# Performance work log

Hardware: AMD Instinct MI355X
Metric: run time of the kernel (lower is better)

## Reference

```python
import jax, jax.numpy as jnp
import numpy as np

B, T, D = 2, 2048, 1024
H, HKV, HD = 16, 4, 64  # num_heads, num_kv_heads, head_dim
EPS = 1.1920929e-07  # torch.finfo(float32).eps, nn.RMSNorm default


def _rmsnorm(x, g):
    return x * jax.lax.rsqrt(jnp.mean(x * x, axis=-1, keepdims=True) + EPS) * g


def _ternary(w):
    # ternary quantize {-1,0,+1} with straight-through estimator
    th = jnp.mean(jnp.abs(w))
    wt = jnp.sign(w) * (jnp.abs(w) > th).astype(w.dtype)
    return w + jax.lax.stop_gradient(wt - w)


def _bitlinear(x, w, g):
    return _rmsnorm(x, g) @ _ternary(w).T


def setup_inputs() -> dict:
    key = jax.random.key(0)
    ks = jax.random.split(key, 5)
    kaiming = lambda k, shape: jax.random.normal(k, shape, jnp.float32) * np.float32(np.sqrt(2.0 / shape[1]))
    return {
        "x": jax.random.normal(ks[0], (B, T, D), jnp.float32),
        "q_w": kaiming(ks[1], (D, D)),
        "q_g": jnp.ones((D,), jnp.float32),
        "k_w": kaiming(ks[2], (HKV * HD, D)),
        "k_g": jnp.ones((D,), jnp.float32),
        "v_w": kaiming(ks[3], (HKV * HD, D)),
        "o_w": kaiming(ks[4], (D, D)),
        "o_g": jnp.ones((D,), jnp.float32),
        "qk_gain": jnp.float32(5.25),
    }


def reference(x, q_w, q_g, k_w, k_g, v_w, o_w, o_g, qk_gain):
    b, t, d = x.shape
    q = _bitlinear(x, q_w, q_g).reshape(b, t, H, HD)          # [B,T,H,hd]
    k = _bitlinear(x, k_w, k_g).reshape(b, t, HKV, HD)        # [B,T,Hkv,hd]
    v = (x @ v_w.T).reshape(b, t, HKV, HD)                    # [B,T,Hkv,hd]
    rep = H // HKV
    k = jnp.repeat(k, rep, axis=2)                            # GQA expand -> [B,T,H,hd]
    v = jnp.repeat(v, rep, axis=2)
    scale = qk_gain / np.float32(np.sqrt(HD))
    attn = jnp.einsum('bqhd,bkhd->bhqk', q, k) * scale        # [B,H,T,T]
    causal = jnp.tril(jnp.ones((t, t), bool))
    attn = jnp.where(causal, attn, -jnp.inf)
    attn = jax.nn.softmax(attn, axis=-1)
    out = jnp.einsum('bhqk,bkhd->bqhd', attn, v).reshape(b, t, d)
    return _bitlinear(out, o_w, o_g)
```

## Files before the change

kernel.cpp:

```cpp
#include <hip/hip_runtime.h>
#include <hip/hip_bf16.h>
#include <cstdint>
#include <cstddef>

typedef unsigned short u16;
typedef unsigned int u32;
typedef __attribute__((ext_vector_type(8))) short short8v;
typedef __attribute__((ext_vector_type(4))) float f32x4;
typedef __attribute__((ext_vector_type(4))) u16 u16x4;
typedef __attribute__((ext_vector_type(8))) u16 u16x8;

static constexpr int Bc = 2, Tc = 2048, Dc = 1024, Hc = 16, HKVc = 4, HDc = 64;
static constexpr int Mc = Bc * Tc;
static constexpr float EPSc = 1.1920929e-07f;

static __device__ __forceinline__ u16 f2bf(float f) {
  u32 u = __builtin_bit_cast(u32, f);
  return (u16)((u + 0x7fffu + ((u >> 16) & 1u)) >> 16);
}
static __device__ __forceinline__ float bf2f(u16 b) {
  u32 u = ((u32)b) << 16;
  return __builtin_bit_cast(float, u);
}
static __device__ __forceinline__ float fast_exp2(float x) {
  float r;
  asm("v_exp_f32 %0, %1" : "=v"(r) : "v"(x));
  return r;
}
static __device__ __forceinline__ u32 cvt_pk_bf16(float lo, float hi) {
  u32 r;
  asm("v_cvt_pk_bf16_f32 %0, %1, %2" : "=v"(r) : "v"(lo), "v"(hi));
  return r;
}

__global__ __launch_bounds__(256) void np_leafsum_all(const float* __restrict__ q_w,
                                                      const float* __restrict__ k_w,
                                                      const float* __restrict__ o_w,
                                                      float* __restrict__ leaf) {
  int blk = blockIdx.x;
  const float* w;
  float* out;
  int lfbase;
  if (blk < 256)      { w = q_w; out = leaf;         lfbase = blk * 32; }
  else if (blk < 320) { w = k_w; out = leaf + 8192;  lfbase = (blk - 256) * 32; }
  else                { w = o_w; out = leaf + 10240; lfbase = (blk - 320) * 32; }
  int t = threadIdx.x;
  int lf = lfbase + (t >> 3), j = t & 7;
  const float* a = w + (size_t)lf * 128;
  float r = fabsf(a[j]);
#pragma unroll
  for (int i = 8; i < 128; i += 8) r += fabsf(a[i + j]);
  float x = r + __shfl_xor(r, 1);
  float y = x + __shfl_xor(x, 2);
  float z = y + __shfl_xor(y, 4);
  if (j == 0) out[lf] = z;
}

__global__ __launch_bounds__(256) void np_treemean3(const float* __restrict__ leaf,
                                                    float* __restrict__ th) {
  int m = blockIdx.x;
  const float* src = leaf + (m == 0 ? 0 : (m == 1 ? 8192 : 10240));
  int nle = (m == 1) ? 2048 : 8192;
  float inv_n = (m == 1) ? (1.0f / 262144.0f) : (1.0f / 1048576.0f);
  int t = threadIdx.x;
  int chunk = nle >> 8;
  float v[32];
  for (int i = 0; i < chunk; i += 4) {
    float4 f = *(const float4*)&src[t * chunk + i];
    v[i] = f.x; v[i + 1] = f.y; v[i + 2] = f.z; v[i + 3] = f.w;
  }
  for (int cnt = chunk >> 1; cnt >= 1; cnt >>= 1)
    for (int i = 0; i < cnt; ++i) v[i] = v[2 * i] + v[2 * i + 1];
  float s = v[0];
#pragma unroll
  for (int off = 1; off < 64; off <<= 1) s += __shfl_xor(s, off);
  __shared__ float red[4];
  if ((t & 63) == 0) red[t >> 6] = s;
  __syncthreads();
  if (t == 0) th[m] = ((red[0] + red[1]) + (red[2] + red[3])) * inv_n;
}

__global__ __launch_bounds__(256) void quant_split_all(const float* __restrict__ q_w,
                                                       const float* __restrict__ k_w,
                                                       const float* __restrict__ o_w,
                                                       const float* __restrict__ v_w,
                                                       const float* __restrict__ th,
                                                       u16* __restrict__ Wq,
                                                       u16* __restrict__ Wk,
                                                       u16* __restrict__ Wo,
                                                       u16* __restrict__ Vwh) {
  int i4 = blockIdx.x * 256 + threadIdx.x;
  if (i4 < 589824) {
    const float* w; u16* o; float t;
    int j;
    if (i4 < 262144)      { w = q_w; o = Wq; t = th[0]; j = i4; }
    else if (i4 < 327680) { w = k_w; o = Wk; t = th[1]; j = i4 - 262144; }
    else                  { w = o_w; o = Wo; t = th[2]; j = i4 - 327680; }
    float4 v = *(const float4*)&w[(size_t)j * 4];
    float y[4] = {v.x, v.y, v.z, v.w};
    u16x4 q;
#pragma unroll
    for (int c = 0; c < 4; ++c)
      q[c] = (y[c] > t) ? (u16)0x3F80 : ((y[c] < -t) ? (u16)0xBF80 : (u16)0);
    *(u16x4*)&o[(size_t)j * 4] = q;
  } else {
    int j = i4 - 589824;
    float4 v = *(const float4*)&v_w[(size_t)j * 4];
    float y[4] = {v.x, v.y, v.z, v.w};
    u16x4 h;
#pragma unroll
    for (int c = 0; c < 4; ++c) h[c] = f2bf(y[c]);
    *(u16x4*)&Vwh[(size_t)j * 4] = h;
  }
}

__global__ __launch_bounds__(256) void rmsnorm_split6(const float* __restrict__ X,
                                                      const float* __restrict__ g1,
                                                      const float* __restrict__ g2,
                                                      u16* __restrict__ H1, u16* __restrict__ L1,
                                                      u16* __restrict__ H2, u16* __restrict__ L2,
                                                      u16* __restrict__ HV) {
  int row = blockIdx.x;
  const float* xr = X + (size_t)row * Dc;
  int tid = threadIdx.x;
  float4 v = *(const float4*)&xr[tid * 4];
  float vv[4] = {v.x, v.y, v.z, v.w};
  if (HV != nullptr) {
    u16x4 h;
#pragma unroll
    for (int j = 0; j < 4; ++j) h[j] = f2bf(vv[j]);
    *(u16x4*)&HV[(size_t)row * Dc + tid * 4] = h;
  }
  float ss = v.x * v.x + v.y * v.y + v.z * v.z + v.w * v.w;
#pragma unroll
  for (int off = 1; off < 64; off <<= 1) ss += __shfl_xor(ss, off);
  __shared__ float red[4];
  if ((tid & 63) == 0) red[tid >> 6] = ss;
  __syncthreads();
  float tot = red[0] + red[1] + red[2] + red[3];
  float inv = 1.0f / sqrtf(tot * (1.0f / (float)Dc) + EPSc);
  {
    float4 a = *(const float4*)&g1[tid * 4];
    float ga[4] = {a.x, a.y, a.z, a.w};
    u16x4 h, l;
#pragma unroll
    for (int j = 0; j < 4; ++j) {
      float y = vv[j] * inv * ga[j];
      u16 hb = f2bf(y);
      h[j] = hb;
      l[j] = f2bf(y - bf2f(hb));
    }
    *(u16x4*)&H1[(size_t)row * Dc + tid * 4] = h;
    if (L1 != nullptr) *(u16x4*)&L1[(size_t)row * Dc + tid * 4] = l;
  }
  if (g2 != nullptr) {
    float4 a = *(const float4*)&g2[tid * 4];
    float ga[4] = {a.x, a.y, a.z, a.w};
    u16x4 h, l;
#pragma unroll
    for (int j = 0; j < 4; ++j) {
      float y = vv[j] * inv * ga[j];
      u16 hb = f2bf(y);
      h[j] = hb;
      l[j] = f2bf(y - bf2f(hb));
    }
    *(u16x4*)&H2[(size_t)row * Dc + tid * 4] = h;
    if (L2 != nullptr) *(u16x4*)&L2[(size_t)row * Dc + tid * 4] = l;
  }
}

template <bool PA, int MODE>
static __device__ __forceinline__ void gemm_body(
    const u16* __restrict__ Ah, const u16* __restrict__ Al,
    const u16* __restrict__ Bh,
    int N, int K, int bm, int bn,
    float* __restrict__ C, u16* __restrict__ O1, u16* __restrict__ O2,
    u16* smem) {
  constexpr int APT = 2, BPT = 4;
  u16* AhS = smem;
  u16* AlS = smem + 4096;
  u16* BhS = smem + 8192;
  int tid = threadIdx.x;
  int l = tid & 63, w = tid >> 6;
  int wm = (w >> 1) * 32, wn = (w & 1) * 64;
  u16x8 rAh[APT], rAl[PA ? APT : 1], rBh[BPT];
  f32x4 acc[2][4] = {};
#define LOADTILE(kb_)                                                               \
  {                                                                                 \
    _Pragma("unroll") for (int p = 0; p < APT; ++p) {                               \
      int idx = tid + p * 256;                                                      \
      int row = idx >> 3, cc = idx & 7;                                             \
      rAh[p] = *(const u16x8*)&Ah[(size_t)(bm + row) * K + (kb_) + cc * 8];         \
      if (PA) rAl[p] = *(const u16x8*)&Al[(size_t)(bm + row) * K + (kb_) + cc * 8]; \
    }                                                                               \
    _Pragma("unroll") for (int p = 0; p < BPT; ++p) {                               \
      int idx = tid + p * 256;                                                      \
      int row = idx >> 3, cc = idx & 7;                                             \
      rBh[p] = *(const u16x8*)&Bh[(size_t)(bn + row) * K + (kb_) + cc * 8];         \
    }                                                                               \
  }
  LOADTILE(0)
  for (int kb = 0; kb < K; kb += 64) {
    __syncthreads();
#pragma unroll
    for (int p = 0; p < APT; ++p) {
      int idx = tid + p * 256;
      int row = idx >> 3, cc = idx & 7;
      int off = row * 64 + ((cc * 8) ^ ((row & 7) << 3));
      *(u16x8*)&AhS[off] = rAh[p];
      if (PA) *(u16x8*)&AlS[off] = rAl[p];
    }
#pragma unroll
    for (int p = 0; p < BPT; ++p) {
      int idx = tid + p * 256;
      int row = idx >> 3, cc = idx & 7;
      int off = row * 64 + ((cc * 8) ^ ((row & 7) << 3));
      *(u16x8*)&BhS[off] = rBh[p];
    }
    if (kb + 64 < K) LOADTILE(kb + 64)
    __syncthreads();
    __builtin_amdgcn_s_setprio(1);
#pragma unroll
    for (int sl = 0; sl < 2; ++sl) {
      short8v fa[2], fal[2], fb[4];
      int kof = (l >> 4) * 8 + sl * 32;
#pragma unroll
      for (int m = 0; m < 2; ++m) {
        int row = wm + m * 16 + (l & 15);
        int off = row * 64 + (kof ^ ((row & 7) << 3));
        fa[m] = *(const short8v*)&AhS[off];
        if (PA) fal[m] = *(const short8v*)&AlS[off];
      }
#pragma unroll
      for (int n = 0; n < 4; ++n) {
        int row = wn + n * 16 + (l & 15);
        int off = row * 64 + (kof ^ ((row & 7) << 3));
        fb[n] = *(const short8v*)&BhS[off];
      }
#pragma unroll
      for (int m = 0; m < 2; ++m)
#pragma unroll
        for (int n = 0; n < 4; ++n) {
          acc[m][n] = __builtin_amdgcn_mfma_f32_16x16x32_bf16(fa[m], fb[n], acc[m][n], 0, 0, 0);
          if (PA)
            acc[m][n] = __builtin_amdgcn_mfma_f32_16x16x32_bf16(fal[m], fb[n], acc[m][n], 0, 0, 0);
        }
    }
    __builtin_amdgcn_s_setprio(0);
  }
#undef LOADTILE
#pragma unroll
  for (int m = 0; m < 2; ++m)
#pragma unroll
    for (int n = 0; n < 4; ++n)
#pragma unroll
      for (int r = 0; r < 4; ++r) {
        int grow = bm + wm + m * 16 + (l >> 4) * 4 + r;
        int gcol = bn + wn + n * 16 + (l & 15);
        float v = acc[m][n][r];
        if (MODE == 0) {
          C[(size_t)grow * N + gcol] = v;
        } else if (MODE == 1) {
          u16 hb = f2bf(v);
          O1[(size_t)grow * N + gcol] = hb;
          O2[(size_t)grow * N + gcol] = f2bf(v - bf2f(hb));
        } else {
          int k = gcol & 31;
          int gp = (gcol & ~31) | (((k >> 2) & 3) << 3) |
                   (((k >> 4) & 1) << 2) | (k & 3);
          O1[(size_t)grow * N + gp] = f2bf(v);
        }
      }
}

__global__ __launch_bounds__(256, 1) void qkv_mega(
    const u16* __restrict__ Xqh, const u16* __restrict__ Xql, const u16* __restrict__ Wq,
    const u16* __restrict__ Xkh, const u16* __restrict__ Xkl, const u16* __restrict__ Wk,
    const u16* __restrict__ Xvh, const u16* __restrict__ Vwh,
    u16* __restrict__ Qh, u16* __restrict__ Ql,
    u16* __restrict__ Kh, u16* __restrict__ Kl,
    u16* __restrict__ Vt) {
  __shared__ __align__(16) u16 SMEM[16384];
  int bx = blockIdx.x;
  if (bx < 512) {
    int bm = (bx >> 3) * 64, bn = (bx & 7) * 128;
    gemm_body<true, 1>(Xqh, Xql, Wq, 1024, 1024, bm, bn, nullptr, Qh, Ql, SMEM);
  } else if (bx < 640) {
    int t = bx - 512;
    int bm = (t >> 1) * 64, bn = (t & 1) * 128;
    gemm_body<true, 1>(Xkh, Xkl, Wk, 256, 1024, bm, bn, nullptr, Kh, Kl, SMEM);
  } else {
    int t = bx - 640;
    int bm = (t >> 5) * 64, bn = (t & 31) * 128;
    gemm_body<false, 3>(Vwh, nullptr, Xvh, 4096, 1024, bm, bn, nullptr, Vt, nullptr, SMEM);
  }
}

__global__ __launch_bounds__(256, 1) void o_gemm(
    const u16* __restrict__ Ah, const u16* __restrict__ Bh,
    float* __restrict__ C) {
  __shared__ __align__(16) u16 SMEM[16384];
  int bm = blockIdx.y * 64, bn = blockIdx.x * 128;
  gemm_body<false, 0>(Ah, nullptr, Bh, 1024, 1024, bm, bn, C, nullptr, nullptr, SMEM);
}

__global__ __launch_bounds__(256, 3) void attn_part(
    const u16* __restrict__ Qh, const u16* __restrict__ Ql,
    const u16* __restrict__ Kh, const u16* __restrict__ Kl,
    const u16* __restrict__ Vt,
    const float* __restrict__ qk_gain,
    u16* __restrict__ Opart, float* __restrict__ MLpart) {
  __shared__ __align__(16) u16 SM[24576];
  int tid = threadIdx.x;
  int w = tid >> 6, l = tid & 63;
  int hb = blockIdx.x;
  int h = hb & 15, b = hb >> 4;
  int kvh = h >> 2;
  int f = blockIdx.y;
  int qt, ci;
  if (f < 4)       { qt = f; ci = 0; }
  else if (f < 12) { int o = f - 4;  qt = 4 + (o >> 1); ci = o & 1; }
  else if (f < 24) { int o = f - 12; qt = 8 + o / 3;    ci = o - (o / 3) * 3; }
  else             { int o = f - 24; qt = 12 + (o >> 2); ci = o & 3; }
  int q0 = qt * 128;
  int tsteps = 2 * qt + 2;
  int s0 = ci * 8;
  int s1 = (s0 + 8 < tsteps) ? (s0 + 8) : tsteps;
  const float sc2 = qk_gain[0] * 0.125f * 1.44269504f;
  u16x8 pk[2], pl[2], pv[2];
#define AISSUE3(K0)                                                             \
  {                                                                             \
    _Pragma("unroll") for (int p = 0; p < 2; ++p) {                             \
      int idx = tid + p * 256;                                                  \
      int jj = idx >> 3, cc = idx & 7;                                          \
      size_t kb = ((size_t)(b * Tc + (K0) + jj)) * (HKVc * HDc) + kvh * 64 + cc * 8; \
      pk[p] = *(const u16x8*)&Kh[kb];                                           \
      pl[p] = *(const u16x8*)&Kl[kb];                                           \
      size_t vb = ((size_t)(kvh * 64 + jj)) * (size_t)Mc + b * Tc + (K0) + cc * 8; \
      pv[p] = *(const u16x8*)&Vt[vb];                                           \
    }                                                                           \
  }
#define WRITEBUF(BI)                                                            \
  {                                                                             \
    u16* bb = SM + (BI) * 12288;                                                \
    _Pragma("unroll") for (int p = 0; p < 2; ++p) {                             \
      int idx = tid + p * 256;                                                  \
      int jj = idx >> 3, cc = idx & 7;                                          \
      int sw = jj * 64 + ((cc * 8) ^ ((jj & 7) << 3));                          \
      *(u16x8*)&bb[sw] = pk[p];                                                 \
      *(u16x8*)&bb[4096 + sw] = pl[p];                                          \
      *(u16x8*)&bb[8192 + sw] = pv[p];                                          \
    }                                                                           \
  }
  short8v qb_h[4], qb_l[4];
#pragma unroll
  for (int qp = 0; qp < 2; ++qp) {
    size_t qrow = (size_t)(b * Tc + q0 + w * 32 + qp * 16 + (l & 15));
#pragma unroll
    for (int sl = 0; sl < 2; ++sl) {
      int dstart = (l >> 4) * 8 + sl * 32;
      qb_h[qp * 2 + sl] = *(const short8v*)&Qh[qrow * Dc + h * 64 + dstart];
      qb_l[qp * 2 + sl] = *(const short8v*)&Ql[qrow * Dc + h * 64 + dstart];
    }
  }
  f32x4 Oacc[8] = {{0,0,0,0},{0,0,0,0},{0,0,0,0},{0,0,0,0},
                   {0,0,0,0},{0,0,0,0},{0,0,0,0},{0,0,0,0}};
  float mrow[2] = {-3.0e38f, -3.0e38f};
  float lrow[2] = {0.f, 0.f};
  int qmax_w = q0 + w * 32 + 31;
  AISSUE3(s0 * 64)
  WRITEBUF(0)
  if (s0 + 1 < s1) AISSUE3((s0 + 1) * 64)
  __syncthreads();
  for (int li = 0; li < s1 - s0; ++li) {
    int stp = s0 + li;
    int k0 = stp * 64;
    u16* Kh_s = SM + (li & 1) * 12288;
    u16* Kl_s = Kh_s + 4096;
    u16* Vt_s = Kh_s + 8192;
    if (stp + 1 < s1) WRITEBUF((li + 1) & 1)
    if (stp + 2 < s1) AISSUE3((stp + 2) * 64)
    if (k0 <= qmax_w) {
      f32x4 s[8] = {{0,0,0,0},{0,0,0,0},{0,0,0,0},{0,0,0,0},
                    {0,0,0,0},{0,0,0,0},{0,0,0,0},{0,0,0,0}};
      __builtin_amdgcn_s_setprio(1);
#pragma unroll
      for (int kt = 0; kt < 4; ++kt) {
        int key = kt * 16 + (l & 15);
#pragma unroll
        for (int sl = 0; sl < 2; ++sl) {
          int dstart = ((l >> 4) * 8 + 32 * sl) ^ ((key & 7) << 3);
          short8v bh = *(const short8v*)&Kh_s[key * 64 + dstart];
          short8v bl = *(const short8v*)&Kl_s[key * 64 + dstart];
#pragma unroll
          for (int qp = 0; qp < 2; ++qp) {
            s[qp * 4 + kt] = __builtin_amdgcn_mfma_f32_16x16x32_bf16(bh, qb_h[qp * 2 + sl], s[qp * 4 + kt], 0, 0, 0);
            s[qp * 4 + kt] = __builtin_amdgcn_mfma_f32_16x16x32_bf16(bl, qb_h[qp * 2 + sl], s[qp * 4 + kt], 0, 0, 0);
            s[qp * 4 + kt] = __builtin_amdgcn_mfma_f32_16x16x32_bf16(bh, qb_l[qp * 2 + sl], s[qp * 4 + kt], 0, 0, 0);
          }
        }
      }
      __builtin_amdgcn_s_setprio(0);
      bool full = (k0 + 63) <= (q0 + w * 32);
      if (!full) {
#pragma unroll
        for (int qp = 0; qp < 2; ++qp) {
          int qg = q0 + w * 32 + qp * 16 + (l & 15);
#pragma unroll
          for (int kt = 0; kt < 4; ++kt)
#pragma unroll
            for (int r = 0; r < 4; ++r)
              if (k0 + kt * 16 + ((l >> 4) << 2) + r > qg) s[qp * 4 + kt][r] = -3.0e38f;
        }
      }
      float p[2][4][4];
#pragma unroll
      for (int qp = 0; qp < 2; ++qp) {
        float mk[4];
#pragma unroll
        for (int kt = 0; kt < 4; ++kt)
          mk[kt] = fmaxf(fmaxf(s[qp * 4 + kt][0], s[qp * 4 + kt][1]),
                         fmaxf(s[qp * 4 + kt][2], s[qp * 4 + kt][3]));
        float mx = fmaxf(fmaxf(mk[0], mk[1]), fmaxf(mk[2], mk[3]));
        mx = fmaxf(mx, __shfl_xor(mx, 16));
        mx = fmaxf(mx, __shfl_xor(mx, 32));
        float mnew = fmaxf(mrow[qp], mx);
        float msc = mnew * sc2;
        float corr = fast_exp2(__builtin_fmaf(mrow[qp], sc2, -msc));
        mrow[qp] = mnew;
        float sk[4];
#pragma unroll
        for (int kt = 0; kt < 4; ++kt) {
#pragma unroll
          for (int r = 0; r < 4; ++r)
            p[qp][kt][r] = fast_exp2(__builtin_fmaf(s[qp * 4 + kt][r], sc2, -msc));
          sk[kt] = (p[qp][kt][0] + p[qp][kt][1]) + (p[qp][kt][2] + p[qp][kt][3]);
        }
        float rs = (sk[0] + sk[1]) + (sk[2] + sk[3]);
        rs += __shfl_xor(rs, 16);
        rs += __shfl_xor(rs, 32);
        lrow[qp] = lrow[qp] * corr + rs;
#pragma unroll
        for (int dt = 0; dt < 4; ++dt) Oacc[qp * 4 + dt] *= corr;
      }
      short8v fbv[4];
#pragma unroll
      for (int qp = 0; qp < 2; ++qp)
#pragma unroll
        for (int sl = 0; sl < 2; ++sl) {
          union { u32 u[4]; short8v v; } fq;
          fq.u[0] = cvt_pk_bf16(p[qp][2 * sl][0], p[qp][2 * sl][1]);
          fq.u[1] = cvt_pk_bf16(p[qp][2 * sl][2], p[qp][2 * sl][3]);
          fq.u[2] = cvt_pk_bf16(p[qp][2 * sl + 1][0], p[qp][2 * sl + 1][1]);
          fq.u[3] = cvt_pk_bf16(p[qp][2 * sl + 1][2], p[qp][2 * sl + 1][3]);
          fbv[qp * 2 + sl] = fq.v;
        }
      __builtin_amdgcn_s_setprio(1);
#pragma unroll
      for (int dt = 0; dt < 4; ++dt) {
        int d = dt * 16 + (l & 15);
#pragma unroll
        for (int sl = 0; sl < 2; ++sl) {
          int kstart = ((l >> 4) * 8 + 32 * sl) ^ ((d & 7) << 3);
          short8v fav = *(const short8v*)&Vt_s[d * 64 + kstart];
#pragma unroll
          for (int qp = 0; qp < 2; ++qp)
            Oacc[qp * 4 + dt] = __builtin_amdgcn_mfma_f32_16x16x32_bf16(fav, fbv[qp * 2 + sl], Oacc[qp * 4 + dt], 0, 0, 0);
        }
      }
      __builtin_amdgcn_s_setprio(0);
    }
    __syncthreads();
  }
  int G = hb * 40 + f;
  u16* Op = Opart + (size_t)G * 8192;
  float* Es = (float*)SM + w * 1088;
#pragma unroll
  for (int qp = 0; qp < 2; ++qp) {
#pragma unroll
    for (int dt = 0; dt < 4; ++dt)
#pragma unroll
      for (int r = 0; r < 4; ++r)
        Es[(l & 15) * 68 + dt * 16 + ((l >> 4) << 2) + r] = Oacc[qp * 4 + dt][r];
    int qloc = w * 32 + qp * 16 + (l >> 2);
#pragma unroll
    for (int j = 0; j < 4; ++j) {
      float4 vv = *(const float4*)&Es[(l >> 2) * 68 + (l & 3) * 4 + j * 16];
      u16x4 o4;
      o4[0] = f2bf(vv.x); o4[1] = f2bf(vv.y); o4[2] = f2bf(vv.z); o4[3] = f2bf(vv.w);
      *(u16x4*)&Op[qloc * 64 + (l & 3) * 4 + j * 16] = o4;
    }
  }
  if (l < 16) {
#pragma unroll
    for (int qp = 0; qp < 2; ++qp) {
      int qloc = w * 32 + qp * 16 + l;
      MLpart[(size_t)G * 256 + qloc * 2 + 0] = mrow[qp];
      MLpart[(size_t)G * 256 + qloc * 2 + 1] = lrow[qp];
    }
  }
#undef AISSUE3
#undef WRITEBUF
}

__global__ __launch_bounds__(256) void attn_merge(const u16* __restrict__ Opart,
                                                  const float* __restrict__ MLpart,
                                                  const float* __restrict__ qk_gain,
                                                  float* __restrict__ AO) {
  int hb = blockIdx.x;
  int h = hb & 15, b = hb >> 4;
  int qt = blockIdx.y;
  int g = qt >> 2, rr = qt & 3;
  int cum = 2 * g * (g + 1) + rr * (g + 1);
  int nc = (2 * qt + 9) >> 3;
  const float sc2 = qk_gain[0] * 0.125f * 1.44269504f;
  int t = threadIdx.x;
  int q = t >> 1, dh = (t & 1) * 32;
  size_t Gbase = (size_t)hb * 40 + cum;
  float mi[4], li[4];
  float M = -3.0e38f;
  for (int i = 0; i < nc; ++i) {
    mi[i] = MLpart[(Gbase + i) * 256 + q * 2 + 0];
    li[i] = MLpart[(Gbase + i) * 256 + q * 2 + 1];
    M = fmaxf(M, mi[i]);
  }
  float acc[32] = {};
  float L = 0.0f;
  for (int i = 0; i < nc; ++i) {
    float wgt = fast_exp2((mi[i] - M) * sc2);
    L += wgt * li[i];
    const u16* Op = Opart + (Gbase + i) * 8192 + q * 64 + dh;
#pragma unroll
    for (int c = 0; c < 4; ++c) {
      u16x8 v8 = *(const u16x8*)&Op[c * 8];
#pragma unroll
      for (int j = 0; j < 8; ++j) acc[c * 8 + j] += wgt * bf2f(v8[j]);
    }
  }
  float inv = 1.0f / L;
  size_t arow = ((size_t)(b * Tc + qt * 128 + q)) * Dc + h * 64 + dh;
#pragma unroll
  for (int c = 0; c < 8; ++c) {
    float4 o = make_float4(acc[c * 4] * inv, acc[c * 4 + 1] * inv,
                           acc[c * 4 + 2] * inv, acc[c * 4 + 3] * inv);
    *(float4*)&AO[arow + c * 4] = o;
  }
}

extern "C" void kernel_launch(void* const* d_in, const int* in_sizes, int n_in,
                              void* d_out, int out_size, void* d_ws, size_t ws_size,
                              hipStream_t stream) {
  const float* x    = (const float*)d_in[0];
  const float* q_w  = (const float*)d_in[1];
  const float* q_g  = (const float*)d_in[2];
  const float* k_w  = (const float*)d_in[3];
  const float* k_g  = (const float*)d_in[4];
  const float* v_w  = (const float*)d_in[5];
  const float* o_w  = (const float*)d_in[6];
  const float* o_g  = (const float*)d_in[7];
  const float* qk_g = (const float*)d_in[8];

  char* base = (char*)d_ws;
  u16* Xqh = (u16*)(base + (0ull  << 20));
  u16* Xql = (u16*)(base + (8ull  << 20));
  u16* Xkh = (u16*)(base + (16ull << 20));
  u16* Xkl = (u16*)(base + (24ull << 20));
  u16* Xvh = (u16*)(base + (32ull << 20));
  u16* Qh  = (u16*)(base + (40ull << 20));
  u16* Ql  = (u16*)(base + (48ull << 20));
  u16* Kh  = (u16*)(base + (56ull << 20));
  u16* Kl  = (u16*)(base + (58ull << 20));
  u16* Vt  = (u16*)(base + (60ull << 20));
  u16* Wq  = (u16*)(base + (62ull << 20));
  u16* Wk  = (u16*)(base + (64ull << 20));
  u16* Wo  = (u16*)(base + (64ull << 20) + (512ull << 10));
  u16* Vwh = (u16*)(base + (66ull << 20) + (512ull << 10));
  float* leaf = (float*)(base + (67ull << 20));
  float* th   = leaf + 18432;
  float* AO     = (float*)base;
  u16*  Opart   = (u16*)(base + (16ull << 20));
  float* MLpart = (float*)(base + (36ull << 20));
  u16*  Xoh     = (u16*)(base + (16ull << 20));

  np_leafsum_all<<<576, 256, 0, stream>>>(q_w, k_w, o_w, leaf);
  np_treemean3<<<3, 256, 0, stream>>>(leaf, th);

  quant_split_all<<<2560, 256, 0, stream>>>(q_w, k_w, o_w, v_w, th, Wq, Wk, Wo, Vwh);

  rmsnorm_split6<<<Mc, 256, 0, stream>>>(x, q_g, k_g, Xqh, Xql, Xkh, Xkl, Xvh);

  qkv_mega<<<768, 256, 0, stream>>>(Xqh, Xql, Wq, Xkh, Xkl, Wk, Xvh, Vwh,
                                    Qh, Ql, Kh, Kl, Vt);

  attn_part<<<dim3(32, 40), 256, 0, stream>>>(Qh, Ql, Kh, Kl, Vt, qk_g, Opart, MLpart);
  attn_merge<<<dim3(32, 16), 256, 0, stream>>>(Opart, MLpart, qk_g, AO);

  rmsnorm_split6<<<Mc, 256, 0, stream>>>(AO, o_g, nullptr, Xoh, nullptr, nullptr, nullptr,
                                         nullptr);
  o_gemm<<<dim3(8, 64), 256, 0, stream>>>(Xoh, Wo, (float*)d_out);
}
```

Baseline: 141.4 us.

## Rebalance attention split to two chunks and fuse merge with output RMSNorm

The causal attention work split changes from up to four fixed 8-step chunks per query tile (40 blocks per head) to 24 blocks per head. The upper eight query tiles are halved into two chunks and the lower eight run unsplit, with heavy tiles scheduled first. The merge kernel is replaced by merge_rms, which combines the at most two partials per row and applies the output RMSNorm in one pass, writing bf16 directly. This removes the fp32 AO round-trip and one kernel launch. Null checks are also dropped from rmsnorm_split6 since its only remaining call passes every pointer.

```diff
diff --git a/kernel.cpp b/kernel.cpp
--- a/kernel.cpp
+++ b/kernel.cpp
@@ -151,9 +151,9 @@
       l[j] = f2bf(y - bf2f(hb));
     }
     *(u16x4*)&H1[(size_t)row * Dc + tid * 4] = h;
-    if (L1 != nullptr) *(u16x4*)&L1[(size_t)row * Dc + tid * 4] = l;
-  }
-  if (g2 != nullptr) {
+    *(u16x4*)&L1[(size_t)row * Dc + tid * 4] = l;
+  }
+  {
     float4 a = *(const float4*)&g2[tid * 4];
     float ga[4] = {a.x, a.y, a.z, a.w};
     u16x4 h, l;
@@ -165,7 +165,7 @@
       l[j] = f2bf(y - bf2f(hb));
     }
     *(u16x4*)&H2[(size_t)row * Dc + tid * 4] = h;
-    if (L2 != nullptr) *(u16x4*)&L2[(size_t)row * Dc + tid * 4] = l;
+    *(u16x4*)&L2[(size_t)row * Dc + tid * 4] = l;
   }
 }
 
@@ -317,15 +317,18 @@
   int h = hb & 15, b = hb >> 4;
   int kvh = h >> 2;
   int f = blockIdx.y;
-  int qt, ci;
-  if (f < 4)       { qt = f; ci = 0; }
-  else if (f < 12) { int o = f - 4;  qt = 4 + (o >> 1); ci = o & 1; }
-  else if (f < 24) { int o = f - 12; qt = 8 + o / 3;    ci = o - (o / 3) * 3; }
-  else             { int o = f - 24; qt = 12 + (o >> 2); ci = o & 3; }
+  int qt, s0, s1;
+  if (f < 16) {
+    qt = 15 - (f >> 1);
+    int half = qt + 1;
+    s0 = (f & 1) * half;
+    s1 = s0 + half;
+  } else {
+    qt = 23 - f;
+    s0 = 0;
+    s1 = 2 * qt + 2;
+  }
   int q0 = qt * 128;
-  int tsteps = 2 * qt + 2;
-  int s0 = ci * 8;
-  int s1 = (s0 + 8 < tsteps) ? (s0 + 8) : tsteps;
   const float sc2 = qk_gain[0] * 0.125f * 1.44269504f;
   u16x8 pk[2], pl[2], pv[2];
 #define AISSUE3(K0)                                                             \
@@ -472,7 +475,7 @@
     }
     __syncthreads();
   }
-  int G = hb * 40 + f;
+  int G = hb * 24 + f;
   u16* Op = Opart + (size_t)G * 8192;
   float* Es = (float*)SM + w * 1088;
 #pragma unroll
@@ -503,48 +506,69 @@
 #undef WRITEBUF
 }
 
-__global__ __launch_bounds__(256) void attn_merge(const u16* __restrict__ Opart,
-                                                  const float* __restrict__ MLpart,
-                                                  const float* __restrict__ qk_gain,
-                                                  float* __restrict__ AO) {
-  int hb = blockIdx.x;
-  int h = hb & 15, b = hb >> 4;
-  int qt = blockIdx.y;
-  int g = qt >> 2, rr = qt & 3;
-  int cum = 2 * g * (g + 1) + rr * (g + 1);
-  int nc = (2 * qt + 9) >> 3;
+__global__ __launch_bounds__(256) void merge_rms(const u16* __restrict__ Opart,
+                                                 const float* __restrict__ MLpart,
+                                                 const float* __restrict__ o_g,
+                                                 const float* __restrict__ qk_gain,
+                                                 u16* __restrict__ Xoh) {
   const float sc2 = qk_gain[0] * 0.125f * 1.44269504f;
   int t = threadIdx.x;
-  int q = t >> 1, dh = (t & 1) * 32;
-  size_t Gbase = (size_t)hb * 40 + cum;
-  float mi[4], li[4];
-  float M = -3.0e38f;
-  for (int i = 0; i < nc; ++i) {
-    mi[i] = MLpart[(Gbase + i) * 256 + q * 2 + 0];
-    li[i] = MLpart[(Gbase + i) * 256 + q * 2 + 1];
-    M = fmaxf(M, mi[i]);
-  }
-  float acc[32] = {};
-  float L = 0.0f;
-  for (int i = 0; i < nc; ++i) {
-    float wgt = fast_exp2((mi[i] - M) * sc2);
-    L += wgt * li[i];
-    const u16* Op = Opart + (Gbase + i) * 8192 + q * 64 + dh;
-#pragma unroll
-    for (int c = 0; c < 4; ++c) {
-      u16x8 v8 = *(const u16x8*)&Op[c * 8];
-#pragma unroll
-      for (int j = 0; j < 8; ++j) acc[c * 8 + j] += wgt * bf2f(v8[j]);
-    }
-  }
-  float inv = 1.0f / L;
-  size_t arow = ((size_t)(b * Tc + qt * 128 + q)) * Dc + h * 64 + dh;
-#pragma unroll
-  for (int c = 0; c < 8; ++c) {
-    float4 o = make_float4(acc[c * 4] * inv, acc[c * 4 + 1] * inv,
-                           acc[c * 4 + 2] * inv, acc[c * 4 + 3] * inv);
-    *(float4*)&AO[arow + c * 4] = o;
-  }
+  int row_i = t >> 6, l = t & 63;
+  int rr = blockIdx.x * 4 + row_i;
+  int b = rr >> 11, tpos = rr & 2047;
+  int qt = tpos >> 7, qloc = tpos & 127;
+  int head = l >> 2;
+  int hb = b * 16 + head;
+  int f0, nc;
+  if (qt >= 8) { f0 = 2 * (15 - qt); nc = 2; }
+  else         { f0 = 23 - qt;       nc = 1; }
+  size_t Gbase = (size_t)hb * 24 + f0;
+  float m0 = MLpart[Gbase * 256 + qloc * 2 + 0];
+  float l0 = MLpart[Gbase * 256 + qloc * 2 + 1];
+  float m1 = -3.0e38f, l1 = 0.0f;
+  if (nc == 2) {
+    m1 = MLpart[(Gbase + 1) * 256 + qloc * 2 + 0];
+    l1 = MLpart[(Gbase + 1) * 256 + qloc * 2 + 1];
+  }
+  float M = fmaxf(m0, m1);
+  float w0 = fast_exp2((m0 - M) * sc2);
+  float w1 = (nc == 2) ? fast_exp2((m1 - M) * sc2) : 0.0f;
+  float L = w0 * l0 + w1 * l1;
+  int dio = (l & 3) * 16;
+  const u16* Op0 = Opart + Gbase * 8192 + qloc * 64 + dio;
+  float val[16];
+  {
+    u16x8 a0 = *(const u16x8*)&Op0[0];
+    u16x8 a1 = *(const u16x8*)&Op0[8];
+#pragma unroll
+    for (int j = 0; j < 8; ++j) { val[j] = w0 * bf2f(a0[j]); val[8 + j] = w0 * bf2f(a1[j]); }
+  }
+  if (nc == 2) {
+    const u16* Op1 = Op0 + 8192;
+    u16x8 a0 = *(const u16x8*)&Op1[0];
+    u16x8 a1 = *(const u16x8*)&Op1[8];
+#pragma unroll
+    for (int j = 0; j < 8; ++j) { val[j] += w1 * bf2f(a0[j]); val[8 + j] += w1 * bf2f(a1[j]); }
+  }
+  float invL = 1.0f / L;
+#pragma unroll
+  for (int j = 0; j < 16; ++j) val[j] *= invL;
+  float ss = 0.0f;
+#pragma unroll
+  for (int j = 0; j < 16; ++j) ss += val[j] * val[j];
+#pragma unroll
+  for (int off = 1; off < 64; off <<= 1) ss += __shfl_xor(ss, off);
+  float inv = 1.0f / sqrtf(ss * (1.0f / (float)Dc) + EPSc);
+  int col = head * 64 + dio;
+  u16x8 h0, h1;
+#pragma unroll
+  for (int j = 0; j < 8; ++j) {
+    h0[j] = f2bf(val[j] * inv * o_g[col + j]);
+    h1[j] = f2bf(val[8 + j] * inv * o_g[col + 8 + j]);
+  }
+  u16* dst = Xoh + (size_t)rr * Dc + col;
+  *(u16x8*)&dst[0] = h0;
+  *(u16x8*)&dst[8] = h1;
 }
 
 extern "C" void kernel_launch(void* const* d_in, const int* in_sizes, int n_in,
@@ -577,10 +601,9 @@
   u16* Vwh = (u16*)(base + (66ull << 20) + (512ull << 10));
   float* leaf = (float*)(base + (67ull << 20));
   float* th   = leaf + 18432;
-  float* AO     = (float*)base;
   u16*  Opart   = (u16*)(base + (16ull << 20));
-  float* MLpart = (float*)(base + (36ull << 20));
-  u16*  Xoh     = (u16*)(base + (16ull << 20));
+  float* MLpart = (float*)(base + (28ull << 20));
+  u16*  Xoh     = (u16*)base;
 
   np_leafsum_all<<<576, 256, 0, stream>>>(q_w, k_w, o_w, leaf);
   np_treemean3<<<3, 256, 0, stream>>>(leaf, th);
@@ -592,10 +615,9 @@
   qkv_mega<<<768, 256, 0, stream>>>(Xqh, Xql, Wq, Xkh, Xkl, Wk, Xvh, Vwh,
                                     Qh, Ql, Kh, Kl, Vt);
 
-  attn_part<<<dim3(32, 40), 256, 0, stream>>>(Qh, Ql, Kh, Kl, Vt, qk_g, Opart, MLpart);
-  attn_merge<<<dim3(32, 16), 256, 0, stream>>>(Opart, MLpart, qk_g, AO);
-
-  rmsnorm_split6<<<Mc, 256, 0, stream>>>(AO, o_g, nullptr, Xoh, nullptr, nullptr, nullptr,
-                                         nullptr);
+  attn_part<<<dim3(32, 24), 256, 0, stream>>>(Qh, Ql, Kh, Kl, Vt, qk_g, Opart, MLpart);
+
+  merge_rms<<<1024, 256, 0, stream>>>(Opart, MLpart, o_g, qk_g, Xoh);
+
   o_gemm<<<dim3(8, 64), 256, 0, stream>>>(Xoh, Wo, (float*)d_out);
 }
```

Result: faster. 133.3 us, median of 2 (-5.8%).
